# Optimization experiments

Hardware: AMD Instinct MI355X
Metric: run time of the kernel (lower is better)

Reference implementation:

```python
import jax, jax.numpy as jnp
import numpy as np

# Dims: batch, in/out channels, spatial grid, pole counts per dim (last halved for rfft)
B, CI, CO = 8, 32, 32
N1, N2 = 256, 256
K1, K2 = 16, 9  # n_modes=(16,16), complex_data=False -> (16, 16//2+1)


def setup_inputs() -> dict:
    key = jax.random.key(0)
    ks = jax.random.split(key, 8)
    std = (2.0 / (CI + CO)) ** 0.5  # init_std='auto'
    s = std / np.sqrt(2.0)          # cfloat randn: real/imag each var 1/2
    return {
        "x": jax.random.normal(ks[0], (B, CI, N1, N2), dtype=jnp.float32),
        "residue_r": s * jax.random.normal(ks[1], (CI, CO, K1, K2), dtype=jnp.float32),
        "residue_i": s * jax.random.normal(ks[2], (CI, CO, K1, K2), dtype=jnp.float32),
        "pole1_r": s * jax.random.normal(ks[3], (CI, CO, K1), dtype=jnp.float32),
        "pole1_i": s * jax.random.normal(ks[4], (CI, CO, K1), dtype=jnp.float32),
        "pole2_r": s * jax.random.normal(ks[5], (CI, CO, K2), dtype=jnp.float32),
        "pole2_i": s * jax.random.normal(ks[6], (CI, CO, K2), dtype=jnp.float32),
        "bias": std * jax.random.normal(ks[7], (CO, 1, 1), dtype=jnp.float32),
    }


def _forward(x, residue_r, residue_i, pole1_r, pole1_i, pole2_r, pole2_i, bias):
    residue = residue_r + 1j * residue_i          # [i,o,k,l] cfloat
    p1 = pole1_r + 1j * pole1_i                   # [i,o,k]
    p2 = pole2_r + 1j * pole2_i                   # [i,o,l]

    # Laplace variable samples lambda = 2*pi*j*f along each dim (grid on [0,1), dt=1/N)
    lam1 = 1j * (2.0 * jnp.pi) * jnp.fft.fftfreq(N1, 1.0 / N1).astype(jnp.float32)    # [N1]
    lam2 = 1j * (2.0 * jnp.pi) * jnp.fft.rfftfreq(N2, 1.0 / N2).astype(jnp.float32)   # [N2//2+1]

    # pole-residue factors 1/(lambda_d - pole_d)
    P1 = 1.0 / (lam1[None, None, None, :] - p1[..., None])   # [i,o,k,x]
    P2 = 1.0 / (lam2[None, None, None, :] - p2[..., None])   # [i,o,l,y]

    # FFT of input (real data -> rfft over trailing dims), forward norm
    alpha = jnp.fft.rfftn(x, axes=(-2, -1), norm="forward")  # [b,i,x,y] c64

    # transient response: Hw(f) = residue * prod_d 1/(lambda_d - pole_d)
    Hw = jnp.einsum("iokl,iokx,ioly->ioxy", residue, P1, P2)   # [i,o,x,y]
    r1 = jnp.einsum("bixy,ioxy->boxy", alpha, Hw)
    x1 = jnp.fft.irfftn(r1, s=(N1, N2), axes=(-2, -1), norm="forward")  # real [b,o,N1,N2]

    # steady-state residues: -sum_f alpha * residue * prod_d P_d, keep (i,k,l)
    r2 = -jnp.einsum("bixy,iokl,iokx,ioly->biokl", alpha, residue, P1, P2)

    t1 = (jnp.arange(N1, dtype=jnp.float32) / N1)
    t2 = (jnp.arange(N2, dtype=jnp.float32) / N2)
    E1 = jnp.exp(p1[..., None] * t1)   # [i,o,k,z]
    E2 = jnp.exp(p2[..., None] * t2)   # [i,o,l,w]
    x2 = jnp.real(jnp.einsum("biokl,iokz,iolw->bozw", r2, E1, E2))  # [b,o,N1,N2]

    return x1 + x2 + bias[None]


def reference(x, residue_r, residue_i, pole1_r, pole1_i, pole2_r, pole2_i, bias):
    return _forward(x, residue_r, residue_i, pole1_r, pole1_i, pole2_r, pole2_i, bias)
```

## Files before the change

kernel.cpp:

```cpp
#include <hip/hip_runtime.h>
#include <math.h>

#define NB 8
#define CIn 32
#define COut 32
#define NIO 1024
#define NN1 256
#define NN2 256
#define NYF 129
#define NK1 16
#define NK2 9
#define NKL 144

typedef float2 c32;
typedef __attribute__((ext_vector_type(8))) __bf16 bf16x8;
typedef __attribute__((ext_vector_type(4))) float f32x4;

__device__ __forceinline__ c32 cadd(c32 a, c32 b){ return make_float2(a.x+b.x, a.y+b.y); }
__device__ __forceinline__ c32 csub(c32 a, c32 b){ return make_float2(a.x-b.x, a.y-b.y); }
__device__ __forceinline__ c32 cmul(c32 a, c32 b){ return make_float2(a.x*b.x - a.y*b.y, a.x*b.y + a.y*b.x); }
__device__ __forceinline__ c32 cfma(c32 a, c32 b, c32 acc){
  acc.x = fmaf(a.x, b.x, acc.x); acc.x = fmaf(-a.y, b.y, acc.x);
  acc.y = fmaf(a.x, b.y, acc.y); acc.y = fmaf(a.y, b.x, acc.y);
  return acc;
}
__device__ __forceinline__ unsigned short f2bf(float f){
  unsigned int u = __float_as_uint(f);
  u += 0x7FFF + ((u >> 16) & 1);
  return (unsigned short)(u >> 16);
}
__device__ __forceinline__ float bf2f(unsigned short h){
  unsigned int u = ((unsigned int)h) << 16;
  return __uint_as_float(u);
}
__device__ __forceinline__ void split_bf(float f, unsigned short& hi, unsigned short& lo){
  hi = f2bf(f);
  lo = f2bf(f - bf2f(hi));
}

#define GLOAD16(lptr, gptr) \
  __builtin_amdgcn_global_load_lds((const __attribute__((address_space(1))) unsigned int*)(gptr), \
                                   (__attribute__((address_space(3))) unsigned int*)(lptr), 16, 0, 0)

template<int INV> __device__ __forceinline__ c32 rot90(c32 a){
  return INV ? make_float2(-a.y, a.x) : make_float2(a.y, -a.x);
}
template<int INV> __device__ __forceinline__ void dft4(c32& a0, c32& a1, c32& a2, c32& a3){
  c32 t0 = cadd(a0,a2), t1 = csub(a0,a2);
  c32 t2 = cadd(a1,a3), t3 = rot90<INV>(csub(a1,a3));
  a0 = cadd(t0,t2); a1 = cadd(t1,t3); a2 = csub(t0,t2); a3 = csub(t1,t3);
}
__device__ __forceinline__ int SLOT16(int k){ return 4*(k&3) + (k>>2); }
template<int INV> __device__ __forceinline__ c32 twg(const float2* ltw, int idx){
  float2 w = ltw[idx & 255];
  return INV ? make_float2(w.x, w.y) : make_float2(w.x, -w.y);
}
template<int INV> __device__ __forceinline__ void fft16r(c32 v[16], const float2* ltw){
#pragma unroll
  for (int bp = 0; bp < 4; bp++) dft4<INV>(v[bp], v[4+bp], v[8+bp], v[12+bp]);
#pragma unroll
  for (int c = 1; c < 4; c++)
#pragma unroll
    for (int bp = 1; bp < 4; bp++)
      v[4*c+bp] = cmul(v[4*c+bp], twg<INV>(ltw, 16*bp*c));
#pragma unroll
  for (int c = 0; c < 4; c++) dft4<INV>(v[4*c], v[4*c+1], v[4*c+2], v[4*c+3]);
}
template<int INV>
__device__ __forceinline__ void fft256_core(c32 v[16], int b, c32* tile, const float2* ltw){
  fft16r<INV>(v, ltw);
#pragma unroll
  for (int c = 0; c < 16; c++){
    c32 g = (c && b) ? cmul(v[SLOT16(c)], twg<INV>(ltw, b*c)) : v[SLOT16(c)];
    tile[c*17 + b] = g;
  }
  __syncthreads();
#pragma unroll
  for (int j = 0; j < 16; j++) v[j] = tile[b*17 + j];
  fft16r<INV>(v, ltw);
}

__global__ void k_tw(float2* __restrict__ tw){
  int m = threadIdx.x;
  double ang = 6.283185307179586 * (double)m / 256.0;
  tw[m] = make_float2((float)cos(ang), (float)sin(ang));
}

__global__ void k_p2(const float* __restrict__ p2r, const float* __restrict__ p2i, c32* __restrict__ P2){
  int idx = blockIdx.x * 256 + threadIdx.x;
  if (idx >= NIO * NYF) return;
  int io = idx / NYF, y = idx - io * NYF;
  c32* row = P2 + (size_t)idx * 10;
#pragma unroll
  for (int l = 0; l < 9; l++){
    float a = -p2r[io*9 + l];
    float b = 6.2831853071795864f * (float)y - p2i[io*9 + l];
    float inv = 1.0f / fmaf(a, a, b * b);
    row[l] = make_float2(a * inv, -b * inv);
  }
}

__global__ void k_e1(const float* __restrict__ p1r, const float* __restrict__ p1i, c32* __restrict__ E1){
  int idx = blockIdx.x * 256 + threadIdx.x;
  int z = idx & 255; int iok = idx >> 8;
  float t = (float)z * (1.0f / 256.0f);
  float er = expf(p1r[iok] * t);
  float s, c; sincosf(p1i[iok] * t, &s, &c);
  E1[idx] = make_float2(er * c, er * s);
}

__global__ __launch_bounds__(256) void k_fwd_y(const float* __restrict__ x, const float2* __restrict__ tw,
                                               c32* __restrict__ alpha){
  __shared__ c32 tile[16*272];
  __shared__ float2 ltw[256];
  int t = threadIdx.x;
  ltw[t] = tw[t];
  int bi = blockIdx.x >> 3;
  int n1c = (blockIdx.x & 7) << 5;
  int row = t >> 4, b = t & 15;
  const float* xe = x + ((size_t)bi * 256 + n1c + 2 * row) * 256;
  c32 v[16];
#pragma unroll
  for (int a = 0; a < 16; a++)
    v[a] = make_float2(xe[16*a + b], xe[256 + 16*a + b]);
  __syncthreads();
  fft256_core<0>(v, b, tile + row*272, ltw);
  __syncthreads();
#pragma unroll
  for (int d = 0; d < 16; d++)
    tile[row*272 + b + 16*d] = v[SLOT16(d)];
  __syncthreads();
  const float sc = 0.5f / 65536.0f;
#pragma unroll
  for (int j = 0; j < 8; j++){
    int item = t + 256*j;
    int h = item & 127, r2 = item >> 7;
    c32* Zb = tile + r2*272;
    if (h == 0){
      c32 z0 = Zb[0], z1 = Zb[128];
      Zb[0]   = make_float2(z0.x * (2.0f*sc), z0.y * (2.0f*sc));
      Zb[128] = make_float2(z1.x * (2.0f*sc), z1.y * (2.0f*sc));
    } else {
      c32 zk = Zb[h], zm = Zb[256 - h];
      c32 A = make_float2(sc*(zk.x + zm.x), sc*(zk.y - zm.y));
      c32 B = make_float2(sc*(zk.y + zm.y), sc*(zm.x - zk.x));
      Zb[h] = A; Zb[256 - h] = B;
    }
  }
  __syncthreads();
  for (int j = 0; j < 17; j++){
    int idx = t + 256*j;
    if (idx >= 129*32) break;
    int y = idx >> 5, n1i = idx & 31;
    c32* Zb = tile + (n1i >> 1)*272;
    c32 val;
    if ((n1i & 1) == 0)
      val = (y == 0) ? make_float2(Zb[0].x, 0.0f)
          : (y == 128) ? make_float2(Zb[128].x, 0.0f) : Zb[y];
    else
      val = (y == 0) ? make_float2(Zb[0].y, 0.0f)
          : (y == 128) ? make_float2(Zb[128].y, 0.0f) : Zb[256 - y];
    alpha[((size_t)bi * 129 + y) * 256 + n1c + n1i] = val;
  }
}

template<int INV>
__global__ __launch_bounds__(256) void k_fft_x(const float2* __restrict__ tw, c32* __restrict__ buf){
  __shared__ c32 tile[16*272];
  __shared__ float2 ltw[256];
  int t = threadIdx.x;
  ltw[t] = tw[t];
  int row = t >> 4, b = t & 15;
  c32* p = buf + ((size_t)blockIdx.x * 16 + row) * 256;
  c32 v[16];
#pragma unroll
  for (int a = 0; a < 16; a++) v[a] = p[16*a + b];
  __syncthreads();
  fft256_core<INV>(v, b, tile + row*272, ltw);
#pragma unroll
  for (int d = 0; d < 16; d++) p[b + 16*d] = v[SLOT16(d)];
}

__global__ __launch_bounds__(256) void k_inv_y(const c32* __restrict__ r1, const float* __restrict__ bias,
                                               const float2* __restrict__ tw, float* __restrict__ out){
  __shared__ c32 tile[16*272];
  __shared__ float2 ltw[256];
  c32* SA = tile;
  int t = threadIdx.x;
  ltw[t] = tw[t];
  int bo = blockIdx.x >> 3;
  int z0 = (blockIdx.x & 7) << 5;
  for (int j = 0; j < 17; j++){
    int idx = t + 256*j;
    if (idx >= 129*32) break;
    int y = idx >> 5, zi = idx & 31;
    SA[y*33 + zi] = r1[((size_t)bo * 129 + y) * 256 + z0 + zi];
  }
  __syncthreads();
  int p = t >> 4, b = t & 15;
  c32 v[16];
#pragma unroll
  for (int a = 0; a < 16; a++){
    int k = 16*a + b;
    int m = (k <= 128) ? k : 256 - k;
    c32 A = SA[m*33 + 2*p], B = SA[m*33 + 2*p + 1];
    if (k == 0 || k == 128)  v[a] = make_float2(A.x, B.x);
    else if (k < 128)        v[a] = make_float2(A.x - B.y, A.y + B.x);
    else                     v[a] = make_float2(A.x + B.y, B.x - A.y);
  }
  __syncthreads();
  fft256_core<1>(v, b, tile + p*272, ltw);
  float bv = bias[bo & 31];
  float* o0 = out + ((size_t)bo * 256 + z0 + 2*p) * 256;
#pragma unroll
  for (int d = 0; d < 16; d++){
    c32 zz = v[SLOT16(d)];
    o0[b + 16*d]       = zz.x + bv;
    o0[256 + b + 16*d] = zz.y + bv;
  }
}

__global__ __launch_bounds__(256, 4) void k_r1(const c32* __restrict__ alpha,
                                               const float* __restrict__ rr, const float* __restrict__ ri,
                                               const float* __restrict__ p1r, const float* __restrict__ p1i,
                                               const c32* __restrict__ P2,
                                               c32* __restrict__ r1){
  __shared__ float4 R2r4[512], R2i4[512];
  int t = threadIdx.x;
  int j = blockIdx.x;
  int g = (j & 7) * 132 + (j >> 3);
  int y4 = g >> 5, o = g & 31;
  int y0 = y4 * 4;
  int yv = (y0 + 4 <= 129) ? 4 : (129 - y0);
  float* R2r = (float*)R2r4; float* R2i = (float*)R2i4;
#pragma unroll
  for (int e = 0; e < 8; e++){
    int flat = t + e * 256;
    int i = flat >> 6, k = (flat >> 2) & 15, yy = flat & 3;
    int io = i * 32 + o;
    int iok = io * 16 + k;
    int ya = y0 + yy; if (ya > 128) ya = 128;
    float ar = 0.f, ai = 0.f;
#pragma unroll
    for (int l = 0; l < 9; l++){
      float rsr = rr[iok*9 + l], rsi = ri[iok*9 + l];
      c32 p2 = P2[((size_t)io * NYF + ya) * 10 + l];
      ar = fmaf(rsr, p2.x, ar); ar = fmaf(-rsi, p2.y, ar);
      ai = fmaf(rsr, p2.y, ai); ai = fmaf(rsi, p2.x, ai);
    }
    R2r[flat] = ar; R2i[flat] = ai;
  }
  __syncthreads();
  int x = t;
  float fx = (x < 128) ? (float)x : (float)(x - 256);
  float lamb = 6.2831853071795864f * fx;
  float acr[8][4], aci[8][4];
#pragma unroll
  for (int b = 0; b < 8; b++)
#pragma unroll
    for (int yy = 0; yy < 4; yy++){ acr[b][yy] = 0.f; aci[b][yy] = 0.f; }
  size_t yoff[4];
#pragma unroll
  for (int yy = 0; yy < 4; yy++){
    int ya = y0 + yy; if (ya > 128) ya = 128;
    yoff[yy] = (size_t)ya * 256;
  }
  for (int i = 0; i < 32; i++){
    int io = i * 32 + o;
    const float* pr = p1r + io * 16;
    const float* pim = p1i + io * 16;
    float hwr[4] = {0.f,0.f,0.f,0.f}, hwi[4] = {0.f,0.f,0.f,0.f};
#pragma unroll
    for (int k = 0; k < 16; k++){
      float a = -pr[k];
      float b = lamb - pim[k];
      float inv = 1.0f / fmaf(a, a, b * b);
      float px = a * inv, py = -b * inv;
      float4 r4 = R2r4[i*16 + k], i4 = R2i4[i*16 + k];
      hwr[0]=fmaf(px,r4.x,hwr[0]); hwr[0]=fmaf(-py,i4.x,hwr[0]);
      hwi[0]=fmaf(px,i4.x,hwi[0]); hwi[0]=fmaf( py,r4.x,hwi[0]);
      hwr[1]=fmaf(px,r4.y,hwr[1]); hwr[1]=fmaf(-py,i4.y,hwr[1]);
      hwi[1]=fmaf(px,i4.y,hwi[1]); hwi[1]=fmaf( py,r4.y,hwi[1]);
      hwr[2]=fmaf(px,r4.z,hwr[2]); hwr[2]=fmaf(-py,i4.z,hwr[2]);
      hwi[2]=fmaf(px,i4.z,hwi[2]); hwi[2]=fmaf( py,r4.z,hwi[2]);
      hwr[3]=fmaf(px,r4.w,hwr[3]); hwr[3]=fmaf(-py,i4.w,hwr[3]);
      hwi[3]=fmaf(px,i4.w,hwi[3]); hwi[3]=fmaf( py,r4.w,hwi[3]);
    }
    const c32* ab = alpha + (size_t)i * 129 * 256 + x;
#pragma unroll
    for (int b = 0; b < 8; b++){
      const c32* ap = ab + (size_t)b * 32 * 129 * 256;
#pragma unroll
      for (int yy = 0; yy < 4; yy++){
        c32 av = ap[yoff[yy]];
        acr[b][yy]=fmaf(av.x,hwr[yy],acr[b][yy]); acr[b][yy]=fmaf(-av.y,hwi[yy],acr[b][yy]);
        aci[b][yy]=fmaf(av.x,hwi[yy],aci[b][yy]); aci[b][yy]=fmaf( av.y,hwr[yy],aci[b][yy]);
      }
    }
  }
#pragma unroll
  for (int b = 0; b < 8; b++)
    for (int yy = 0; yy < yv; yy++)
      r1[(((size_t)(b*32 + o) * 129) + y0 + yy) * 256 + x] = make_float2(acr[b][yy], aci[b][yy]);
}

__global__ __launch_bounds__(256) void k_r2k(const c32* __restrict__ alpha,
                                             const float* __restrict__ p1r, const float* __restrict__ p1i,
                                             const c32* __restrict__ P2,
                                             const float* __restrict__ rr, const float* __restrict__ ri,
                                             c32* __restrict__ r2){
  __shared__ c32 Ts[256 * 12];
  int t = threadIdx.x;
  int j = blockIdx.x;
  int bid = (j & 7) * 1024 + (j >> 3);
  int o = bid & 31; int bi = bid >> 5;
  int i = bi & 31;  int b = bi >> 5;
  int io = i * COut + o;
  {
    float tr[9], ti[9];
#pragma unroll
    for (int l = 0; l < 9; l++){ tr[l] = 0.f; ti[l] = 0.f; }
    const c32* ap = alpha + (size_t)bi * NYF * 256 + t;
    const float* __restrict__ P2u = (const float*)(P2 + (size_t)io * NYF * 10);
    c32 a0 = ap[0], a1 = ap[256], a2 = ap[512], a3 = ap[768];
#define R2K_BODY(aa, Y, PF) { \
      const float* prw = P2u + (size_t)(Y) * 20; \
      float axr = (aa).x, ayi = (aa).y; \
      PF; \
      _Pragma("unroll") \
      for (int l = 0; l < 9; l++){ \
        float pc = prw[2*l], ps = prw[2*l+1]; \
        tr[l] = fmaf(axr, pc, tr[l]); tr[l] = fmaf(-ayi, ps, tr[l]); \
        ti[l] = fmaf(axr, ps, ti[l]); ti[l] = fmaf(ayi, pc, ti[l]); } }
    for (int yb = 0; yb < 128; yb += 4){
      R2K_BODY(a0, yb+0, a0 = ap[(size_t)(yb+4)*256]);
      R2K_BODY(a1, yb+1, a1 = ap[(size_t)(yb+5)*256]);
      R2K_BODY(a2, yb+2, a2 = ap[(size_t)(yb+6)*256]);
      R2K_BODY(a3, yb+3, a3 = ap[(size_t)(yb+7)*256]);
    }
    R2K_BODY(a0, 128, );
#undef R2K_BODY
    c32* myrow = Ts + t * 12;
#pragma unroll
    for (int l = 0; l < 9; l++) myrow[l] = make_float2(tr[l], ti[l]);
  }
  __syncthreads();
  {
    int k = t >> 4, c = t & 15;
    float pa = -p1r[io*16 + k];
    float pb =  p1i[io*16 + k];
    float gr[9], gi[9];
#pragma unroll
    for (int l = 0; l < 9; l++){ gr[l] = 0.f; gi[l] = 0.f; }
#pragma unroll 4
    for (int jj = 0; jj < 16; jj++){
      int xx = c + 16*jj;
      float fx = (xx < 128) ? (float)xx : (float)(xx - 256);
      float bb = 6.2831853071795864f * fx - pb;
      float inv = 1.0f / fmaf(pa, pa, bb * bb);
      float px = pa * inv, py = -bb * inv;
      const c32* trow = Ts + xx * 12;
      float4 q0 = *(const float4*)(trow + 0);
      float4 q1 = *(const float4*)(trow + 2);
      float4 q2 = *(const float4*)(trow + 4);
      float4 q3 = *(const float4*)(trow + 6);
      c32    q4 = trow[8];
      float Trv[9] = {q0.x, q0.z, q1.x, q1.z, q2.x, q2.z, q3.x, q3.z, q4.x};
      float Tiv[9] = {q0.y, q0.w, q1.y, q1.w, q2.y, q2.w, q3.y, q3.w, q4.y};
#pragma unroll
      for (int l = 0; l < 9; l++){
        gr[l] = fmaf(px, Trv[l], gr[l]); gr[l] = fmaf(-py, Tiv[l], gr[l]);
        gi[l] = fmaf(px, Tiv[l], gi[l]); gi[l] = fmaf( py, Trv[l], gi[l]);
      }
    }
#pragma unroll
    for (int s = 1; s < 16; s <<= 1){
#pragma unroll
      for (int l = 0; l < 9; l++){
        gr[l] += __shfl_xor(gr[l], s, 64);
        gi[l] += __shfl_xor(gi[l], s, 64);
      }
    }
    if (c == 0){
#pragma unroll
      for (int l = 0; l < 9; l++){
        float resr = rr[(io*16 + k)*9 + l];
        float resi = ri[(io*16 + k)*9 + l];
        r2[((size_t)b * NIO + io) * NKL + k*9 + l] =
          make_float2(-(resr*gr[l] - resi*gi[l]), -(resr*gi[l] + resi*gr[l]));
      }
    }
  }
}

__global__ __launch_bounds__(256) void k_e2b(const float* __restrict__ p2r, const float* __restrict__ p2i,
                                             unsigned int* __restrict__ B){
  int j = blockIdx.x;
  int o = j & 31, ic = j >> 5;
  int w = threadIdx.x;
  float tt = (float)w * (1.0f / 256.0f);
  unsigned int* brow = B + ((size_t)o * 256 + w) * 576;
#pragma unroll
  for (int ii = 0; ii < 4; ii++){
    int i = ic * 4 + ii;
    int io = i * 32 + o;
#pragma unroll
    for (int l = 0; l < 9; l++){
      float pr = p2r[io*9 + l], pi = p2i[io*9 + l];
      float er = expf(pr * tt);
      float s, c; sincosf(pi * tt, &s, &c);
      float vr = er * c, vi = -er * s;
      unsigned short rh, rl, ih, il;
      split_bf(vr, rh, rl); split_bf(vi, ih, il);
      brow[i*9 + l]       = (unsigned int)rh | ((unsigned int)ih << 16);
      brow[288 + i*9 + l] = (unsigned int)rl | ((unsigned int)il << 16);
    }
  }
}

__global__ __launch_bounds__(256) void k_v(const c32* __restrict__ r2, const c32* __restrict__ E1,
                                           unsigned int* __restrict__ Ahi, unsigned int* __restrict__ Alo){
  int t = threadIdx.x;
  int j = blockIdx.x;
  int o = j & 31;
  int rest = j >> 5;
  int b = rest & 7, ic = rest >> 3;
  size_t rowoff = ((size_t)o * 2048 + b * 256 + t) * 288;
  unsigned int* AH = Ahi + rowoff;
  unsigned int* AL = Alo + rowoff;
#pragma unroll 1
  for (int ii = 0; ii < 8; ii++){
    int i = ic * 8 + ii;
    int io = i * 32 + o;
    const c32* e1p = E1 + (size_t)io * 16 * 256 + t;
    c32 e[16];
#pragma unroll
    for (int k = 0; k < 16; k++) e[k] = e1p[(size_t)k * 256];
    const c32* rp = r2 + ((size_t)b * NIO + io) * NKL;
#pragma unroll
    for (int l = 0; l < 9; l++){
      c32 acc = make_float2(0.0f, 0.0f);
#pragma unroll
      for (int k = 0; k < 16; k++) acc = cfma(rp[k*9 + l], e[k], acc);
      unsigned short rh, rl, ih, il;
      split_bf(acc.x, rh, rl); split_bf(acc.y, ih, il);
      AH[i*9 + l] = (unsigned int)rh | ((unsigned int)ih << 16);
      AL[i*9 + l] = (unsigned int)rl | ((unsigned int)il << 16);
    }
  }
}

#define ALO_H 37748736u
__global__ __launch_bounds__(256) void k_x2m(const unsigned short* __restrict__ A,
                                             const unsigned short* __restrict__ B,
                                             float* __restrict__ out){
  __shared__ __align__(16) unsigned short At[128*32];
  __shared__ __align__(16) unsigned short Bt[128*32];
  int t = threadIdx.x;
  int j = blockIdx.x;
  int orig = (j & 7) * 128 + (j >> 3);
  int o  = orig >> 5;
  int mb = (orig >> 1) & 15;
  int nb = orig & 1;
  const unsigned short* Ab = A + ((size_t)o*2048 + mb*128 + (t>>2))*576 + (t&3)*8;
  const unsigned short* Bb = B + ((size_t)o*256  + nb*128 + (t>>2))*1152 + (t&3)*8;
  int ln = t & 63;
  int wm = t >> 7, wn = (t >> 6) & 1;
  int lrow = ln & 15, lk = (ln >> 4) * 8;
  f32x4 acc[4][4];
#pragma unroll
  for (int mi = 0; mi < 4; mi++)
#pragma unroll
    for (int ni = 0; ni < 4; ni++) acc[mi][ni] = (f32x4){0.f,0.f,0.f,0.f};

  for (int ks = 0; ks < 54; ks++){
    int kA = ks % 18;
    int kB = ks % 36;
    const unsigned short* Ap = Ab + (ks >= 36 ? (size_t)ALO_H : 0) + (size_t)kA*32;
    __syncthreads();
    GLOAD16(At + (size_t)t*8,        Ap);
    GLOAD16(At + 2048 + (size_t)t*8, Ap + (size_t)64*576);
    GLOAD16(Bt + (size_t)t*8,        Bb + (size_t)kB*32);
    GLOAD16(Bt + 2048 + (size_t)t*8, Bb + (size_t)kB*32 + (size_t)64*1152);
    __syncthreads();
    bf16x8 av[4], bv[4];
#pragma unroll
    for (int mi = 0; mi < 4; mi++)
      av[mi] = *(const bf16x8*)(At + (wm*64 + mi*16 + lrow)*32 + lk);
#pragma unroll
    for (int ni = 0; ni < 4; ni++)
      bv[ni] = *(const bf16x8*)(Bt + (wn*64 + ni*16 + lrow)*32 + lk);
#pragma unroll
    for (int mi = 0; mi < 4; mi++)
#pragma unroll
      for (int ni = 0; ni < 4; ni++)
        acc[mi][ni] = __builtin_amdgcn_mfma_f32_16x16x32_bf16(av[mi], bv[ni], acc[mi][ni], 0, 0, 0);
  }
  int nglob = nb*128 + wn*64 + (ln & 15);
#pragma unroll
  for (int mi = 0; mi < 4; mi++){
#pragma unroll
    for (int r = 0; r < 4; r++){
      int m = mb*128 + wm*64 + mi*16 + (ln >> 4)*4 + r;
      int b = m >> 8, z = m & 255;
      float* op = out + (((size_t)(b*32 + o) * 256 + z) * 256) + nglob;
#pragma unroll
      for (int ni = 0; ni < 4; ni++)
        op[ni*16] += acc[mi][ni][r];
    }
  }
}

extern "C" void kernel_launch(void* const* d_in, const int* in_sizes, int n_in,
                              void* d_out, int out_size, void* d_ws, size_t ws_size,
                              hipStream_t stream){
  const float* x    = (const float*)d_in[0];
  const float* rr   = (const float*)d_in[1];
  const float* ri   = (const float*)d_in[2];
  const float* p1r  = (const float*)d_in[3];
  const float* p1i  = (const float*)d_in[4];
  const float* p2r  = (const float*)d_in[5];
  const float* p2i  = (const float*)d_in[6];
  const float* bias = (const float*)d_in[7];
  float* out = (float*)d_out;

  char* ws = (char*)d_ws;
  size_t off = 0;
  c32* alpha = (c32*)(ws + off); off += (size_t)NB * CIn * NYF * NN1 * sizeof(c32);
  c32* r1b   = (c32*)(ws + off); off += (size_t)NB * COut * NYF * NN1 * sizeof(c32);
  off += (size_t)NIO * NK1 * NN1 * sizeof(c32);
  c32* P2b   = (c32*)(ws + off); off += (size_t)NIO * NYF * 10 * sizeof(c32);
  off += (size_t)NIO * NK1 * NYF * sizeof(c32) - (size_t)NIO * NYF * 10 * sizeof(c32)
       + (size_t)NIO * NK2 * NYF * sizeof(c32);
  c32* E1b   = (c32*)(ws + off); off += (size_t)NIO * NK1 * NN1 * sizeof(c32);
  c32* r2b   = (c32*)(ws + off); off += (size_t)NB * NIO * NKL * sizeof(c32);
  float2* tw = (float2*)(ws + off); off += 256 * sizeof(float2);
  unsigned short* Abf  = (unsigned short*)(ws + 0);
  unsigned short* E2bf = (unsigned short*)(ws + 150994944);

  k_tw<<<1, 256, 0, stream>>>(tw);
  k_p2<<<(NIO * NYF + 255) / 256, 256, 0, stream>>>(p2r, p2i, P2b);
  k_e1<<<NIO * NK1, 256, 0, stream>>>(p1r, p1i, E1b);

  k_fwd_y<<<NB * CIn * 8, 256, 0, stream>>>(x, tw, alpha);
  k_fft_x<0><<<NB * CIn * NYF / 16, 256, 0, stream>>>(tw, alpha);

  k_r1<<<1056, 256, 0, stream>>>(alpha, rr, ri, p1r, p1i, P2b, r1b);
  k_r2k<<<NB * CIn * COut, 256, 0, stream>>>(alpha, p1r, p1i, P2b, rr, ri, r2b);

  k_fft_x<1><<<NB * COut * NYF / 16, 256, 0, stream>>>(tw, r1b);
  k_inv_y<<<NB * COut * 8, 256, 0, stream>>>(r1b, bias, tw, out);

  k_e2b<<<256, 256, 0, stream>>>(p2r, p2i, (unsigned int*)E2bf);
  k_v<<<1024, 256, 0, stream>>>(r2b, E1b, (unsigned int*)Abf, (unsigned int*)(Abf + ALO_H));
  k_x2m<<<1024, 256, 0, stream>>>(Abf, E2bf, out);
}
```

Baseline: 1.040 ms.

## Retile r1 kernel to 2x2 x/y per thread and use fast reciprocal

Reorganizes the r1 kernel so each thread computes two adjacent x frequencies for two y rows instead of one x for four y rows. Alpha loads and r1 stores become 16-byte vector accesses, and the per-k pole reciprocal is shared across fewer y values. Every exact division in the pole-factor computations across the kernels is replaced by the hardware approximate reciprocal, which cuts division cost but may reduce accuracy slightly.

```diff
diff --git a/kernel.cpp b/kernel.cpp
--- a/kernel.cpp
+++ b/kernel.cpp
@@ -37,6 +37,7 @@
   hi = f2bf(f);
   lo = f2bf(f - bf2f(hi));
 }
+__device__ __forceinline__ float frcp(float x){ return __builtin_amdgcn_rcpf(x); }
 
 #define GLOAD16(lptr, gptr) \
   __builtin_amdgcn_global_load_lds((const __attribute__((address_space(1))) unsigned int*)(gptr), \
@@ -95,7 +96,7 @@
   for (int l = 0; l < 9; l++){
     float a = -p2r[io*9 + l];
     float b = 6.2831853071795864f * (float)y - p2i[io*9 + l];
-    float inv = 1.0f / fmaf(a, a, b * b);
+    float inv = frcp(fmaf(a, a, b * b));
     row[l] = make_float2(a * inv, -b * inv);
   }
 }
@@ -225,83 +226,107 @@
                                                const float* __restrict__ p1r, const float* __restrict__ p1i,
                                                const c32* __restrict__ P2,
                                                c32* __restrict__ r1){
-  __shared__ float4 R2r4[512], R2i4[512];
+  __shared__ float4 R2h[2][512];
   int t = threadIdx.x;
   int j = blockIdx.x;
   int g = (j & 7) * 132 + (j >> 3);
   int y4 = g >> 5, o = g & 31;
   int y0 = y4 * 4;
-  int yv = (y0 + 4 <= 129) ? 4 : (129 - y0);
-  float* R2r = (float*)R2r4; float* R2i = (float*)R2i4;
-#pragma unroll
-  for (int e = 0; e < 8; e++){
+#pragma unroll
+  for (int e = 0; e < 2; e++){
     int flat = t + e * 256;
-    int i = flat >> 6, k = (flat >> 2) & 15, yy = flat & 3;
+    int i = flat >> 4, k = flat & 15;
     int io = i * 32 + o;
     int iok = io * 16 + k;
-    int ya = y0 + yy; if (ya > 128) ya = 128;
-    float ar = 0.f, ai = 0.f;
+    float ar[4] = {0.f,0.f,0.f,0.f}, ai[4] = {0.f,0.f,0.f,0.f};
 #pragma unroll
     for (int l = 0; l < 9; l++){
       float rsr = rr[iok*9 + l], rsi = ri[iok*9 + l];
-      c32 p2 = P2[((size_t)io * NYF + ya) * 10 + l];
-      ar = fmaf(rsr, p2.x, ar); ar = fmaf(-rsi, p2.y, ar);
-      ai = fmaf(rsr, p2.y, ai); ai = fmaf(rsi, p2.x, ai);
-    }
-    R2r[flat] = ar; R2i[flat] = ai;
-  }
-  __syncthreads();
-  int x = t;
-  float fx = (x < 128) ? (float)x : (float)(x - 256);
-  float lamb = 6.2831853071795864f * fx;
-  float acr[8][4], aci[8][4];
+#pragma unroll
+      for (int yy = 0; yy < 4; yy++){
+        int ya = y0 + yy; if (ya > 128) ya = 128;
+        c32 p2 = P2[((size_t)io * NYF + ya) * 10 + l];
+        ar[yy] = fmaf(rsr, p2.x, ar[yy]); ar[yy] = fmaf(-rsi, p2.y, ar[yy]);
+        ai[yy] = fmaf(rsr, p2.y, ai[yy]); ai[yy] = fmaf( rsi, p2.x, ai[yy]);
+      }
+    }
+    R2h[0][flat] = make_float4(ar[0], ar[1], ai[0], ai[1]);
+    R2h[1][flat] = make_float4(ar[2], ar[3], ai[2], ai[3]);
+  }
+  __syncthreads();
+  int xp = t & 127, yh = t >> 7;
+  int x0 = 2 * xp;
+  int yA = y0 + 2 * yh;
+  int yAc = (yA     > 128) ? 128 : yA;
+  int yBc = (yA + 1 > 128) ? 128 : yA + 1;
+  bool wA = (yA     <= 128);
+  bool wB = (yA + 1 <= 128);
+  float fx0 = (x0     < 128) ? (float)x0       : (float)(x0 - 256);
+  float fx1 = (x0 + 1 < 128) ? (float)(x0 + 1) : (float)(x0 + 1 - 256);
+  float lam0 = 6.2831853071795864f * fx0;
+  float lam1 = 6.2831853071795864f * fx1;
+  const float4* __restrict__ R2u = R2h[yh];
+  float acr[8][2][2], aci[8][2][2];
 #pragma unroll
   for (int b = 0; b < 8; b++)
 #pragma unroll
-    for (int yy = 0; yy < 4; yy++){ acr[b][yy] = 0.f; aci[b][yy] = 0.f; }
-  size_t yoff[4];
-#pragma unroll
-  for (int yy = 0; yy < 4; yy++){
-    int ya = y0 + yy; if (ya > 128) ya = 128;
-    yoff[yy] = (size_t)ya * 256;
-  }
+    for (int yy = 0; yy < 2; yy++){
+      acr[b][yy][0] = 0.f; acr[b][yy][1] = 0.f;
+      aci[b][yy][0] = 0.f; aci[b][yy][1] = 0.f;
+    }
+  size_t yoffA = (size_t)yAc * 256, yoffB = (size_t)yBc * 256;
   for (int i = 0; i < 32; i++){
     int io = i * 32 + o;
     const float* pr = p1r + io * 16;
     const float* pim = p1i + io * 16;
-    float hwr[4] = {0.f,0.f,0.f,0.f}, hwi[4] = {0.f,0.f,0.f,0.f};
+    float hwr[2][2] = {{0.f,0.f},{0.f,0.f}};
+    float hwi[2][2] = {{0.f,0.f},{0.f,0.f}};
 #pragma unroll
     for (int k = 0; k < 16; k++){
       float a = -pr[k];
-      float b = lamb - pim[k];
-      float inv = 1.0f / fmaf(a, a, b * b);
-      float px = a * inv, py = -b * inv;
-      float4 r4 = R2r4[i*16 + k], i4 = R2i4[i*16 + k];
-      hwr[0]=fmaf(px,r4.x,hwr[0]); hwr[0]=fmaf(-py,i4.x,hwr[0]);
-      hwi[0]=fmaf(px,i4.x,hwi[0]); hwi[0]=fmaf( py,r4.x,hwi[0]);
-      hwr[1]=fmaf(px,r4.y,hwr[1]); hwr[1]=fmaf(-py,i4.y,hwr[1]);
-      hwi[1]=fmaf(px,i4.y,hwi[1]); hwi[1]=fmaf( py,r4.y,hwi[1]);
-      hwr[2]=fmaf(px,r4.z,hwr[2]); hwr[2]=fmaf(-py,i4.z,hwr[2]);
-      hwi[2]=fmaf(px,i4.z,hwi[2]); hwi[2]=fmaf( py,r4.z,hwi[2]);
-      hwr[3]=fmaf(px,r4.w,hwr[3]); hwr[3]=fmaf(-py,i4.w,hwr[3]);
-      hwi[3]=fmaf(px,i4.w,hwi[3]); hwi[3]=fmaf( py,r4.w,hwi[3]);
-    }
-    const c32* ab = alpha + (size_t)i * 129 * 256 + x;
+      float b0 = lam0 - pim[k];
+      float b1 = lam1 - pim[k];
+      float inv0 = frcp(fmaf(a, a, b0 * b0));
+      float inv1 = frcp(fmaf(a, a, b1 * b1));
+      float px0 = a * inv0, py0 = -b0 * inv0;
+      float px1 = a * inv1, py1 = -b1 * inv1;
+      float4 q = R2u[i*16 + k];
+      hwr[0][0] = fmaf(px0, q.x, hwr[0][0]); hwr[0][0] = fmaf(-py0, q.z, hwr[0][0]);
+      hwi[0][0] = fmaf(px0, q.z, hwi[0][0]); hwi[0][0] = fmaf( py0, q.x, hwi[0][0]);
+      hwr[0][1] = fmaf(px1, q.x, hwr[0][1]); hwr[0][1] = fmaf(-py1, q.z, hwr[0][1]);
+      hwi[0][1] = fmaf(px1, q.z, hwi[0][1]); hwi[0][1] = fmaf( py1, q.x, hwi[0][1]);
+      hwr[1][0] = fmaf(px0, q.y, hwr[1][0]); hwr[1][0] = fmaf(-py0, q.w, hwr[1][0]);
+      hwi[1][0] = fmaf(px0, q.w, hwi[1][0]); hwi[1][0] = fmaf( py0, q.y, hwi[1][0]);
+      hwr[1][1] = fmaf(px1, q.y, hwr[1][1]); hwr[1][1] = fmaf(-py1, q.w, hwr[1][1]);
+      hwi[1][1] = fmaf(px1, q.w, hwi[1][1]); hwi[1][1] = fmaf( py1, q.y, hwi[1][1]);
+    }
+    const c32* ab = alpha + (size_t)i * 129 * 256 + x0;
 #pragma unroll
     for (int b = 0; b < 8; b++){
       const c32* ap = ab + (size_t)b * 32 * 129 * 256;
-#pragma unroll
-      for (int yy = 0; yy < 4; yy++){
-        c32 av = ap[yoff[yy]];
-        acr[b][yy]=fmaf(av.x,hwr[yy],acr[b][yy]); acr[b][yy]=fmaf(-av.y,hwi[yy],acr[b][yy]);
-        aci[b][yy]=fmaf(av.x,hwi[yy],aci[b][yy]); aci[b][yy]=fmaf( av.y,hwr[yy],aci[b][yy]);
-      }
-    }
-  }
-#pragma unroll
-  for (int b = 0; b < 8; b++)
-    for (int yy = 0; yy < yv; yy++)
-      r1[(((size_t)(b*32 + o) * 129) + y0 + yy) * 256 + x] = make_float2(acr[b][yy], aci[b][yy]);
+      float4 vA = *(const float4*)(ap + yoffA);
+      float4 vB = *(const float4*)(ap + yoffB);
+      acr[b][0][0]=fmaf(vA.x,hwr[0][0],acr[b][0][0]); acr[b][0][0]=fmaf(-vA.y,hwi[0][0],acr[b][0][0]);
+      aci[b][0][0]=fmaf(vA.x,hwi[0][0],aci[b][0][0]); aci[b][0][0]=fmaf( vA.y,hwr[0][0],aci[b][0][0]);
+      acr[b][0][1]=fmaf(vA.z,hwr[0][1],acr[b][0][1]); acr[b][0][1]=fmaf(-vA.w,hwi[0][1],acr[b][0][1]);
+      aci[b][0][1]=fmaf(vA.z,hwi[0][1],aci[b][0][1]); aci[b][0][1]=fmaf( vA.w,hwr[0][1],aci[b][0][1]);
+      acr[b][1][0]=fmaf(vB.x,hwr[1][0],acr[b][1][0]); acr[b][1][0]=fmaf(-vB.y,hwi[1][0],acr[b][1][0]);
+      aci[b][1][0]=fmaf(vB.x,hwi[1][0],aci[b][1][0]); aci[b][1][0]=fmaf( vB.y,hwr[1][0],aci[b][1][0]);
+      acr[b][1][1]=fmaf(vB.z,hwr[1][1],acr[b][1][1]); acr[b][1][1]=fmaf(-vB.w,hwi[1][1],acr[b][1][1]);
+      aci[b][1][1]=fmaf(vB.z,hwi[1][1],aci[b][1][1]); aci[b][1][1]=fmaf( vB.w,hwr[1][1],aci[b][1][1]);
+    }
+  }
+#pragma unroll
+  for (int b = 0; b < 8; b++){
+    if (wA){
+      float4 st = make_float4(acr[b][0][0], aci[b][0][0], acr[b][0][1], aci[b][0][1]);
+      *(float4*)(r1 + (((size_t)(b*32 + o) * 129) + yA) * 256 + x0) = st;
+    }
+    if (wB){
+      float4 st = make_float4(acr[b][1][0], aci[b][1][0], acr[b][1][1], aci[b][1][1]);
+      *(float4*)(r1 + (((size_t)(b*32 + o) * 129) + yA + 1) * 256 + x0) = st;
+    }
+  }
 }
 
 __global__ __launch_bounds__(256) void k_r2k(const c32* __restrict__ alpha,
@@ -357,7 +382,7 @@
       int xx = c + 16*jj;
       float fx = (xx < 128) ? (float)xx : (float)(xx - 256);
       float bb = 6.2831853071795864f * fx - pb;
-      float inv = 1.0f / fmaf(pa, pa, bb * bb);
+      float inv = frcp(fmaf(pa, pa, bb * bb));
       float px = pa * inv, py = -bb * inv;
       const c32* trow = Ts + xx * 12;
       float4 q0 = *(const float4*)(trow + 0);
```

Measured after the change: 928.4 us. 10.7% less time.
